# Optimization experiments

Measured on AMD Instinct MI355X. Metric: run time of the kernel, lower is better.

Reference implementation:

```python
import jax, jax.numpy as jnp
import numpy as np
from jax import lax

B, C, H, W, K = 32, 128, 56, 56, 5
CR = C // 4          # reduced channels in weight-gen MLP
CE = 4 * C           # expanded channels
EPS = 1e-6


def setup_inputs() -> dict:
    key = jax.random.key(0)
    ks = jax.random.split(key, 8)
    s = lambda fan: 1.0 / np.sqrt(fan)
    return {
        "x": jax.random.normal(ks[0], (B, C, H, W), jnp.float32),
        "w_fc1": jax.random.normal(ks[1], (CR, C), jnp.float32) * s(C),
        "ln1_w": jnp.ones((CR,), jnp.float32),
        "ln1_b": jnp.zeros((CR,), jnp.float32),
        "w_fc2": jax.random.normal(ks[2], (C * K * K, CR), jnp.float32) * s(CR),
        "ln2_w": jnp.ones((C,), jnp.float32),
        "ln2_b": jnp.zeros((C,), jnp.float32),
        "w_expand": jax.random.normal(ks[3], (CE, C), jnp.float32) * s(C),
        "w_shrink": jax.random.normal(ks[4], (C, CE), jnp.float32) * s(CE),
        "grn_gamma": jax.random.normal(ks[5], (CE,), jnp.float32) * 0.1,
        "grn_beta": jax.random.normal(ks[6], (CE,), jnp.float32) * 0.1,
    }


def _ln(v, w, b, axis):
    u = v.mean(axis, keepdims=True)
    s2 = jnp.square(v - u).mean(axis, keepdims=True)
    return (v - u) * lax.rsqrt(s2 + EPS) * w + b


def reference(x, w_fc1, ln1_w, ln1_b, w_fc2, ln2_w, ln2_b, w_expand, w_shrink,
              grn_gamma, grn_beta):
    b, c, h, w = x.shape
    # ---- dynamic weight generation: pool -> fc1 -> LN -> fc2 ----
    pooled = x.mean((2, 3))                                  # [B, C]
    hdn = pooled @ w_fc1.T                                   # [B, CR]
    hdn = _ln(hdn, ln1_w, ln1_b, axis=-1)                    # channels_first LN over CR
    dyn = hdn @ w_fc2.T                                      # [B, C*K*K]
    dyn_w = dyn.reshape(b * c, 1, K, K)                      # per-sample depthwise kernels
    # ---- per-sample dynamic depthwise conv (groups = B*C) ----
    pad = K // 2
    out = lax.conv_general_dilated(
        x.reshape(1, b * c, h, w), dyn_w,
        window_strides=(1, 1), padding=[(pad, pad), (pad, pad)],
        dimension_numbers=("NCHW", "OIHW", "NCHW"),
        feature_group_count=b * c,
    ).reshape(b, c, h, w)
    # ---- LN (channels_first) over channel dim ----
    u = out.mean(1, keepdims=True)
    s2 = jnp.square(out - u).mean(1, keepdims=True)
    out = (out - u) * lax.rsqrt(s2 + EPS)
    out = ln2_w[None, :, None, None] * out + ln2_b[None, :, None, None]
    # ---- expand 1x1 -> GELU -> GRN -> shrink 1x1 ----
    out = jnp.einsum("bchw,oc->bohw", out, w_expand)         # [B, 4C, H, W]
    out = jax.nn.gelu(out, approximate=False)
    gx = jnp.sqrt(jnp.sum(jnp.square(out), axis=(2, 3), keepdims=True))  # [B,4C,1,1]
    nx = gx / (gx.mean(1, keepdims=True) + EPS)
    g = grn_gamma[None, :, None, None]
    bt = grn_beta[None, :, None, None]
    out = g * (out * nx) + bt + out
    out = jnp.einsum("bohw,co->bchw", out, w_shrink)         # [B, C, H, W]
    return out + x
```

## Files before the change

### kernel.cpp

```cpp
#include <hip/hip_runtime.h>
#include <hip/hip_bf16.h>

#define B_   32
#define C_   128
#define H_   56
#define W_   56
#define HW_  (H_*W_)
#define BHW_ (B_*HW_)
#define K5_  5
#define KK_  25
#define CR_  32
#define CE_  512
#define EPS_ 1e-6f

typedef __hip_bfloat16 bf16;
typedef __attribute__((ext_vector_type(8))) short short8;
typedef __attribute__((ext_vector_type(4))) float f32x4;


__device__ __forceinline__ float wave_reduce_sum(float v) {
#pragma unroll
  for (int off = 32; off > 0; off >>= 1) v += __shfl_down(v, off, 64);
  return v;
}
__device__ __forceinline__ float bf2f(unsigned short u) {
  return __uint_as_float(((unsigned)u) << 16);
}
__device__ __forceinline__ unsigned short f2bf_bits(float f) {
  bf16 h = __float2bfloat16(f);
  unsigned short u;
  __builtin_memcpy(&u, &h, 2);
  return u;
}
__device__ __forceinline__ float fast_gelu(float v) {
  float t = __expf(-1.702f * v);
  return v * __builtin_amdgcn_rcpf(1.0f + t);
}

__global__ __launch_bounds__(256) void prep_kernel(const float* __restrict__ we,
                                                   bf16* __restrict__ weB) {
  int i = blockIdx.x * 256 + threadIdx.x;
  if (i < CE_ * C_) weB[i] = __float2bfloat16(we[i]);
}

__global__ __launch_bounds__(256) void pool_kernel(const float* __restrict__ x,
                                                   float* __restrict__ pooled) {
  int bc = blockIdx.x;
  const float* xp = x + (size_t)bc * HW_;
  float s = 0.f;
  for (int i = threadIdx.x; i < HW_; i += 256) s += xp[i];
  s = wave_reduce_sum(s);
  __shared__ float red[4];
  int lane = threadIdx.x & 63, wid = threadIdx.x >> 6;
  if (lane == 0) red[wid] = s;
  __syncthreads();
  if (threadIdx.x == 0) pooled[bc] = (red[0] + red[1] + red[2] + red[3]) * (1.0f / HW_);
}

__global__ __launch_bounds__(256) void fc_kernel(const float* __restrict__ pooled,
                                                 const float* __restrict__ w_fc1,
                                                 const float* __restrict__ ln1_w,
                                                 const float* __restrict__ ln1_b,
                                                 const float* __restrict__ w_fc2,
                                                 float* __restrict__ dyn) {
  int b = blockIdx.x;
  int tid = threadIdx.x;
  __shared__ float sp[C_];
  __shared__ float sh[CR_];
  __shared__ float shn[CR_];
  __shared__ float stats[2];
  if (tid < C_) sp[tid] = pooled[b * C_ + tid];
  __syncthreads();
  if (tid < CR_) {
    float acc = 0.f;
    const float* wr = w_fc1 + tid * C_;
#pragma unroll 4
    for (int c = 0; c < C_; ++c) acc += sp[c] * wr[c];
    sh[tid] = acc;
  }
  __syncthreads();
  if (tid == 0) {
    float u = 0.f;
    for (int j = 0; j < CR_; ++j) u += sh[j];
    u *= (1.0f / CR_);
    float v = 0.f;
    for (int j = 0; j < CR_; ++j) { float d = sh[j] - u; v += d * d; }
    v *= (1.0f / CR_);
    stats[0] = u;
    stats[1] = rsqrtf(v + EPS_);
  }
  __syncthreads();
  if (tid < CR_) shn[tid] = (sh[tid] - stats[0]) * stats[1] * ln1_w[tid] + ln1_b[tid];
  __syncthreads();
  for (int i = tid; i < C_ * KK_; i += 256) {
    const float* wr = w_fc2 + i * CR_;
    float acc = 0.f;
#pragma unroll
    for (int j = 0; j < CR_; ++j) acc += shn[j] * wr[j];
    dyn[b * (C_ * KK_) + i] = acc;
  }
}

__global__ __launch_bounds__(256) void conv_kernel(const float* __restrict__ x,
                                                   const float* __restrict__ dyn,
                                                   bf16* __restrict__ z) {
  int bc = blockIdx.x;
  int b = bc >> 7;
  int c = bc & 127;
  int tid = threadIdx.x;
  __shared__ float xs[(H_ + 4) * 64];
  __shared__ float wks[KK_];
  {
    int r = tid >> 6;
    int rr = (r < 2) ? r : (56 + r);
    xs[rr * 64 + (tid & 63)] = 0.f;
  }
  if (tid < 224) {
    int r = tid >> 2, q = tid & 3;
    int col = (q < 2) ? q : (56 + q);
    xs[(r + 2) * 64 + col] = 0.f;
  }
  if (tid < KK_) wks[tid] = dyn[b * (C_ * KK_) + c * KK_ + tid];
  const float4* xp4 = reinterpret_cast<const float4*>(x + (size_t)bc * HW_);
  for (int i = tid; i < 784; i += 256) {
    float4 v = xp4[i];
    int h = i / 14, w4 = (i % 14) * 4;
    float* dst = &xs[(h + 2) * 64 + 2 + w4];
    dst[0] = v.x; dst[1] = v.y; dst[2] = v.z; dst[3] = v.w;
  }
  __syncthreads();
  float wr[KK_];
#pragma unroll
  for (int j = 0; j < KK_; ++j) wr[j] = wks[j];
  for (int g = tid; g < 784; g += 256) {
    int h = g / 14;
    int w4 = (g % 14) * 4;
    float a0 = 0.f, a1 = 0.f, a2 = 0.f, a3 = 0.f;
#pragma unroll
    for (int dh = 0; dh < K5_; ++dh) {
      const float* row = &xs[(h + dh) * 64 + w4];
      float4 va = *reinterpret_cast<const float4*>(row);
      float4 vb = *reinterpret_cast<const float4*>(row + 4);
      float v0 = va.x, v1 = va.y, v2 = va.z, v3 = va.w;
      float v4 = vb.x, v5 = vb.y, v6 = vb.z, v7 = vb.w;
      float u0 = wr[dh * 5 + 0], u1 = wr[dh * 5 + 1], u2 = wr[dh * 5 + 2];
      float u3 = wr[dh * 5 + 3], u4 = wr[dh * 5 + 4];
      a0 += v0 * u0 + v1 * u1 + v2 * u2 + v3 * u3 + v4 * u4;
      a1 += v1 * u0 + v2 * u1 + v3 * u2 + v4 * u3 + v5 * u4;
      a2 += v2 * u0 + v3 * u1 + v4 * u2 + v5 * u3 + v6 * u4;
      a3 += v3 * u0 + v4 * u1 + v5 * u2 + v6 * u3 + v7 * u4;
    }
    size_t base = (size_t)bc * HW_ + h * W_ + w4;
    ushort4 pk = make_ushort4(f2bf_bits(a0), f2bf_bits(a1), f2bf_bits(a2), f2bf_bits(a3));
    *reinterpret_cast<ushort4*>(reinterpret_cast<unsigned short*>(z) + base) = pk;
  }
}

__global__ __launch_bounds__(256) void ln_kernel(const bf16* __restrict__ z,
                                                 const float* __restrict__ ln2_w,
                                                 const float* __restrict__ ln2_b,
                                                 bf16* __restrict__ yT) {
  int hw0 = blockIdx.x * 64;
  int b = blockIdx.y;
  int tid = threadIdx.x;
  int wq = tid & 63;
  int cq = tid >> 6;
  __shared__ unsigned short zt[C_][64];
  __shared__ unsigned short yt[64][136];
  __shared__ float redS[4][64];
  __shared__ float redQ[4][64];
  __shared__ float meanArr[64];
  __shared__ float invArr[64];
  float s = 0.f, q = 0.f;
  const unsigned short* zp = reinterpret_cast<const unsigned short*>(z);
#pragma unroll 4
  for (int k = 0; k < 32; ++k) {
    int c = cq * 32 + k;
    unsigned short u = zp[((size_t)(b * C_ + c)) * HW_ + hw0 + wq];
    float v = bf2f(u);
    s += v;
    q += v * v;
    zt[c][wq] = u;
  }
  redS[cq][wq] = s;
  redQ[cq][wq] = q;
  __syncthreads();
  if (cq == 0) {
    float ss = redS[0][wq] + redS[1][wq] + redS[2][wq] + redS[3][wq];
    float qq = redQ[0][wq] + redQ[1][wq] + redQ[2][wq] + redQ[3][wq];
    float m = ss * (1.0f / C_);
    float var = qq * (1.0f / C_) - m * m;
    meanArr[wq] = m;
    invArr[wq] = rsqrtf(fmaxf(var, 0.f) + EPS_);
  }
  __syncthreads();
  float m = meanArr[wq], iv = invArr[wq];
#pragma unroll
  for (int g = 0; g < 4; ++g) {
    unsigned short pk[8];
#pragma unroll
    for (int i = 0; i < 8; ++i) {
      int c = cq * 32 + g * 8 + i;
      float v = bf2f(zt[c][wq]);
      pk[i] = f2bf_bits((v - m) * iv * ln2_w[c] + ln2_b[c]);
    }
    int4 t;
    __builtin_memcpy(&t, pk, 16);
    *reinterpret_cast<int4*>(&yt[wq][cq * 32 + g * 8]) = t;
  }
  __syncthreads();
  unsigned short* yp = reinterpret_cast<unsigned short*>(yT);
#pragma unroll
  for (int i = 0; i < 4; ++i) {
    int t = tid + 256 * i;
    int row = t >> 4, ch = t & 15;
    int4 v = *reinterpret_cast<const int4*>(&yt[row][ch * 8]);
    *reinterpret_cast<int4*>(yp + ((size_t)(b * HW_ + hw0 + row)) * C_ + ch * 8) = v;
  }
}

__global__ __launch_bounds__(256, 4) void expand_mfma(const bf16* __restrict__ yT,
                                                      const bf16* __restrict__ weB,
                                                      bf16* __restrict__ eT,
                                                      float* __restrict__ gx2) {
  int j0 = blockIdx.x * 128;
  int o0 = blockIdx.y * 128;
  int tid = threadIdx.x;
  int lane = tid & 63, wid = tid >> 6;
  int wm = wid >> 1, wn = wid & 1;
  int quad = lane >> 4, l15 = lane & 15;
  __shared__ __align__(16) char smem[128 * 136 * 2];
  short (*As)[40] = reinterpret_cast<short(*)[40]>(&smem[0]);
  short (*Bs)[40] = reinterpret_cast<short(*)[40]>(&smem[10240]);
  f32x4 acc[4][4] = {};
  const short* yTs = reinterpret_cast<const short*>(yT);
  const short* weS = reinterpret_cast<const short*>(weB);
  for (int k0 = 0; k0 < C_; k0 += 32) {
#pragma unroll
    for (int t = tid; t < 512; t += 256) {
      int r = t >> 2, ch = t & 3;
      int4 va = *reinterpret_cast<const int4*>(yTs + (size_t)(j0 + r) * C_ + k0 + ch * 8);
      *reinterpret_cast<int4*>(&As[r][ch * 8]) = va;
      int4 vb = *reinterpret_cast<const int4*>(weS + (size_t)(o0 + r) * C_ + k0 + ch * 8);
      *reinterpret_cast<int4*>(&Bs[r][ch * 8]) = vb;
    }
    __syncthreads();
    short8 a[4], bfr[4];
#pragma unroll
    for (int mf = 0; mf < 4; ++mf)
      a[mf] = *reinterpret_cast<const short8*>(&As[wm * 64 + mf * 16 + l15][quad * 8]);
#pragma unroll
    for (int nf = 0; nf < 4; ++nf)
      bfr[nf] = *reinterpret_cast<const short8*>(&Bs[wn * 64 + nf * 16 + l15][quad * 8]);
#pragma unroll
    for (int mf = 0; mf < 4; ++mf)
#pragma unroll
      for (int nf = 0; nf < 4; ++nf)
        acc[mf][nf] = __builtin_amdgcn_mfma_f32_16x16x32_bf16(a[mf], bfr[nf], acc[mf][nf], 0, 0, 0);
    __syncthreads();
  }
  short (*Es)[136] = reinterpret_cast<short(*)[136]>(&smem[0]);
#pragma unroll
  for (int mf = 0; mf < 4; ++mf) {
    int jm = j0 + wm * 64 + mf * 16;
    int bb = jm / HW_;
    int jrow = wm * 64 + mf * 16 + quad * 4;
#pragma unroll
    for (int nf = 0; nf < 4; ++nf) {
      int oc = wn * 64 + nf * 16 + l15;
      float g2 = 0.f;
#pragma unroll
      for (int r = 0; r < 4; ++r) {
        float ge = fast_gelu(acc[mf][nf][r]);
        g2 += ge * ge;
        Es[jrow + r][oc] = (short)f2bf_bits(ge);
      }
      g2 += __shfl_xor(g2, 16, 64);
      g2 += __shfl_xor(g2, 32, 64);
      if (quad == 0) atomicAdd(&gx2[bb * CE_ + o0 + oc], g2);
    }
  }
  __syncthreads();
  unsigned short* eP = reinterpret_cast<unsigned short*>(eT);
#pragma unroll
  for (int i = 0; i < 8; ++i) {
    int t = tid + 256 * i;
    int row = t >> 4, ch = t & 15;
    int4 v = *reinterpret_cast<const int4*>(&Es[row][ch * 8]);
    *reinterpret_cast<int4*>(eP + (size_t)(j0 + row) * CE_ + o0 + ch * 8) = v;
  }
}

__global__ __launch_bounds__(512) void grn_scale_kernel(const float* __restrict__ gx2,
                                                        const float* __restrict__ gamma,
                                                        float* __restrict__ scale) {
  int b = blockIdx.x;
  int o = threadIdx.x;
  float gx = sqrtf(gx2[b * CE_ + o]);
  float s = wave_reduce_sum(gx);
  __shared__ float red[8];
  __shared__ float meansh;
  int lane = o & 63, wid = o >> 6;
  if (lane == 0) red[wid] = s;
  __syncthreads();
  if (o == 0) {
    float t = 0.f;
    for (int i = 0; i < 8; ++i) t += red[i];
    meansh = t * (1.0f / CE_);
  }
  __syncthreads();
  scale[b * CE_ + o] = 1.0f + gamma[o] * (gx / (meansh + EPS_));
}

__global__ __launch_bounds__(128) void sb_kernel(const float* __restrict__ w_shrink,
                                                 const float* __restrict__ beta,
                                                 float* __restrict__ sb) {
  int c = threadIdx.x;
  float acc = 0.f;
  for (int o = 0; o < CE_; ++o) acc += w_shrink[c * CE_ + o] * beta[o];
  sb[c] = acc;
}

__global__ __launch_bounds__(256) void scale_ws_kernel(const float* __restrict__ ws,
                                                       const float* __restrict__ scale,
                                                       bf16* __restrict__ sws) {
  int c = blockIdx.x;
  int b = blockIdx.y;
  const float* sp = scale + b * CE_;
  const float* wp = ws + (size_t)c * CE_;
  bf16* op = sws + ((size_t)(b * C_ + c)) * CE_;
  for (int i = threadIdx.x; i < CE_; i += 256)
    op[i] = __float2bfloat16(wp[i] * sp[i]);
}

__global__ __launch_bounds__(256, 4) void shrink_mfma(const bf16* __restrict__ eT,
                                                      const bf16* __restrict__ sws,
                                                      const float* __restrict__ sb,
                                                      const float* __restrict__ x,
                                                      float* __restrict__ out) {
  int hw0 = blockIdx.x * 128;
  int b = blockIdx.y;
  int tid = threadIdx.x;
  int lane = tid & 63, wid = tid >> 6;
  int wm = wid >> 1, wn = wid & 1;
  int quad = lane >> 4, l15 = lane & 15;
  __shared__ __align__(16) char smem[64 * 136 * 4];
  short (*As)[40] = reinterpret_cast<short(*)[40]>(&smem[0]);
  short (*Bs)[40] = reinterpret_cast<short(*)[40]>(&smem[10240]);
  f32x4 acc[4][4] = {};
  const short* eS = reinterpret_cast<const short*>(eT) + (size_t)b * HW_ * CE_;
  const short* wsS = reinterpret_cast<const short*>(sws) + (size_t)b * C_ * CE_;
  for (int k0 = 0; k0 < CE_; k0 += 32) {
#pragma unroll
    for (int t = tid; t < 512; t += 256) {
      int r = t >> 2, ch = t & 3;
      int hwc = hw0 + r; if (hwc >= HW_) hwc = HW_ - 1;
      int4 va = *reinterpret_cast<const int4*>(eS + (size_t)hwc * CE_ + k0 + ch * 8);
      *reinterpret_cast<int4*>(&As[r][ch * 8]) = va;
      int4 vb = *reinterpret_cast<const int4*>(wsS + (size_t)r * CE_ + k0 + ch * 8);
      *reinterpret_cast<int4*>(&Bs[r][ch * 8]) = vb;
    }
    __syncthreads();
    short8 a[4], bfr[4];
#pragma unroll
    for (int mf = 0; mf < 4; ++mf)
      a[mf] = *reinterpret_cast<const short8*>(&As[wm * 64 + mf * 16 + l15][quad * 8]);
#pragma unroll
    for (int nf = 0; nf < 4; ++nf)
      bfr[nf] = *reinterpret_cast<const short8*>(&Bs[wn * 64 + nf * 16 + l15][quad * 8]);
#pragma unroll
    for (int mf = 0; mf < 4; ++mf)
#pragma unroll
      for (int nf = 0; nf < 4; ++nf)
        acc[mf][nf] = __builtin_amdgcn_mfma_f32_16x16x32_bf16(a[mf], bfr[nf], acc[mf][nf], 0, 0, 0);
    __syncthreads();
  }
  float (*Ef)[136] = reinterpret_cast<float(*)[136]>(&smem[0]);
#pragma unroll
  for (int phase = 0; phase < 2; ++phase) {
    if (wn == phase) {
#pragma unroll
      for (int mf = 0; mf < 4; ++mf) {
        int hwr = wm * 64 + mf * 16 + quad * 4;
#pragma unroll
        for (int nf = 0; nf < 4; ++nf) {
          int cr = nf * 16 + l15;
          *reinterpret_cast<f32x4*>(&Ef[cr][hwr]) = acc[mf][nf];
        }
      }
    }
    __syncthreads();
#pragma unroll
    for (int i = 0; i < 8; ++i) {
      int t = tid + 256 * i;
      int row = t >> 5, ch = t & 31;
      int hw = hw0 + ch * 4;
      if (hw < HW_) {
        int c = phase * 64 + row;
        size_t base = ((size_t)(b * C_ + c)) * HW_ + hw;
        float add = sb[c];
        f32x4 av = *reinterpret_cast<const f32x4*>(&Ef[row][ch * 4]);
        float4 xv = *reinterpret_cast<const float4*>(x + base);
        float4 ov;
        ov.x = av.x + add + xv.x;
        ov.y = av.y + add + xv.y;
        ov.z = av.z + add + xv.z;
        ov.w = av.w + add + xv.w;
        *reinterpret_cast<float4*>(out + base) = ov;
      }
    }
    __syncthreads();
  }
}

extern "C" void kernel_launch(void* const* d_in, const int* in_sizes, int n_in,
                              void* d_out, int out_size, void* d_ws, size_t ws_size,
                              hipStream_t stream) {
  (void)in_sizes; (void)n_in; (void)out_size; (void)ws_size;
  const float* x        = (const float*)d_in[0];
  const float* w_fc1    = (const float*)d_in[1];
  const float* ln1_w    = (const float*)d_in[2];
  const float* ln1_b    = (const float*)d_in[3];
  const float* w_fc2    = (const float*)d_in[4];
  const float* ln2_w    = (const float*)d_in[5];
  const float* ln2_b    = (const float*)d_in[6];
  const float* w_expand = (const float*)d_in[7];
  const float* w_shrink = (const float*)d_in[8];
  const float* gamma    = (const float*)d_in[9];
  const float* beta     = (const float*)d_in[10];
  float* out = (float*)d_out;

  char* ws = (char*)d_ws;
  float* pooled = (float*)(ws + 0);
  float* dyn    = (float*)(ws + 16384);
  float* gx2    = (float*)(ws + 425984);
  float* scale  = (float*)(ws + 491520);
  float* sb     = (float*)(ws + 557056);
  bf16*  weB    = (bf16*)(ws + 557568);
  bf16*  yT     = (bf16*)(ws + 819712);
  bf16*  sws    = (bf16*)(ws + 819712);
  bf16*  eT     = (bf16*)(ws + 26509824);
  bf16*  z      = eT;

  prep_kernel<<<256, 256, 0, stream>>>(w_expand, weB);
  pool_kernel<<<B_ * C_, 256, 0, stream>>>(x, pooled);
  fc_kernel<<<B_, 256, 0, stream>>>(pooled, w_fc1, ln1_w, ln1_b, w_fc2, dyn);
  conv_kernel<<<B_ * C_, 256, 0, stream>>>(x, dyn, z);
  ln_kernel<<<dim3(49, B_), 256, 0, stream>>>(z, ln2_w, ln2_b, yT);
  hipMemsetAsync(gx2, 0, B_ * CE_ * sizeof(float), stream);
  expand_mfma<<<dim3(784, 4), 256, 0, stream>>>(yT, weB, eT, gx2);
  grn_scale_kernel<<<B_, 512, 0, stream>>>(gx2, gamma, scale);
  sb_kernel<<<1, 128, 0, stream>>>(w_shrink, beta, sb);
  scale_ws_kernel<<<dim3(C_, B_), 256, 0, stream>>>(w_shrink, scale, sws);
  shrink_mfma<<<dim3(25, B_), 256, 0, stream>>>(eT, sws, sb, x, out);
}
```

Baseline: 297.4 us.

## Recompute expand GEMM in fused shrink to avoid materializing expanded activations

Replaces the expand GEMM that wrote the full bf16 expanded tensor with a GEMM pass that only accumulates GRN sum-of-squares. A fused shrink kernel then recomputes the expand GEMM per tile, applies GELU and the GRN scale, stages the result in shared memory and feeds it straight into the shrink GEMM. This removes the large write and read of the 4C expanded intermediate and the per-batch scaled shrink-weight kernel, at the cost of running the expand GEMM twice. Fragments are loaded directly from global memory rather than staged through LDS, and the sb kernel is parallelized across blocks.

```diff
diff --git a/kernel.cpp b/kernel.cpp
--- a/kernel.cpp
+++ b/kernel.cpp
@@ -38,9 +38,12 @@
 }
 
 __global__ __launch_bounds__(256) void prep_kernel(const float* __restrict__ we,
-                                                   bf16* __restrict__ weB) {
+                                                   const float* __restrict__ ws,
+                                                   bf16* __restrict__ weB,
+                                                   bf16* __restrict__ wsB) {
   int i = blockIdx.x * 256 + threadIdx.x;
   if (i < CE_ * C_) weB[i] = __float2bfloat16(we[i]);
+  else              wsB[i - CE_ * C_] = __float2bfloat16(ws[i - CE_ * C_]);
 }
 
 __global__ __launch_bounds__(256) void pool_kernel(const float* __restrict__ x,
@@ -219,75 +222,55 @@
   }
 }
 
-__global__ __launch_bounds__(256, 4) void expand_mfma(const bf16* __restrict__ yT,
-                                                      const bf16* __restrict__ weB,
-                                                      bf16* __restrict__ eT,
-                                                      float* __restrict__ gx2) {
+__global__ __launch_bounds__(256, 2) void gx2_pass(const bf16* __restrict__ yT,
+                                                   const bf16* __restrict__ weB,
+                                                   float* __restrict__ gx2) {
   int j0 = blockIdx.x * 128;
-  int o0 = blockIdx.y * 128;
   int tid = threadIdx.x;
   int lane = tid & 63, wid = tid >> 6;
   int wm = wid >> 1, wn = wid & 1;
   int quad = lane >> 4, l15 = lane & 15;
-  __shared__ __align__(16) char smem[128 * 136 * 2];
-  short (*As)[40] = reinterpret_cast<short(*)[40]>(&smem[0]);
-  short (*Bs)[40] = reinterpret_cast<short(*)[40]>(&smem[10240]);
-  f32x4 acc[4][4] = {};
-  const short* yTs = reinterpret_cast<const short*>(yT);
+  const short* yS = reinterpret_cast<const short*>(yT);
   const short* weS = reinterpret_cast<const short*>(weB);
-  for (int k0 = 0; k0 < C_; k0 += 32) {
-#pragma unroll
-    for (int t = tid; t < 512; t += 256) {
-      int r = t >> 2, ch = t & 3;
-      int4 va = *reinterpret_cast<const int4*>(yTs + (size_t)(j0 + r) * C_ + k0 + ch * 8);
-      *reinterpret_cast<int4*>(&As[r][ch * 8]) = va;
-      int4 vb = *reinterpret_cast<const int4*>(weS + (size_t)(o0 + r) * C_ + k0 + ch * 8);
-      *reinterpret_cast<int4*>(&Bs[r][ch * 8]) = vb;
-    }
-    __syncthreads();
-    short8 a[4], bfr[4];
+  short8 afr[4][4];
+#pragma unroll
+  for (int ks = 0; ks < 4; ++ks)
 #pragma unroll
     for (int mf = 0; mf < 4; ++mf)
-      a[mf] = *reinterpret_cast<const short8*>(&As[wm * 64 + mf * 16 + l15][quad * 8]);
-#pragma unroll
-    for (int nf = 0; nf < 4; ++nf)
-      bfr[nf] = *reinterpret_cast<const short8*>(&Bs[wn * 64 + nf * 16 + l15][quad * 8]);
-#pragma unroll
-    for (int mf = 0; mf < 4; ++mf)
+      afr[ks][mf] = *reinterpret_cast<const short8*>(
+          yS + (size_t)(j0 + wm * 64 + mf * 16 + l15) * C_ + ks * 32 + quad * 8);
+#pragma unroll 1
+  for (int n = 0; n < 4; ++n) {
+    int oc0 = n * 128;
+    f32x4 acc[4][4] = {};
+#pragma unroll
+    for (int ks = 0; ks < 4; ++ks) {
+      short8 bfr[4];
 #pragma unroll
       for (int nf = 0; nf < 4; ++nf)
-        acc[mf][nf] = __builtin_amdgcn_mfma_f32_16x16x32_bf16(a[mf], bfr[nf], acc[mf][nf], 0, 0, 0);
-    __syncthreads();
-  }
-  short (*Es)[136] = reinterpret_cast<short(*)[136]>(&smem[0]);
-#pragma unroll
-  for (int mf = 0; mf < 4; ++mf) {
-    int jm = j0 + wm * 64 + mf * 16;
-    int bb = jm / HW_;
-    int jrow = wm * 64 + mf * 16 + quad * 4;
+        bfr[nf] = *reinterpret_cast<const short8*>(
+            weS + (size_t)(oc0 + wn * 64 + nf * 16 + l15) * C_ + ks * 32 + quad * 8);
+#pragma unroll
+      for (int mf = 0; mf < 4; ++mf)
+#pragma unroll
+        for (int nf = 0; nf < 4; ++nf)
+          acc[mf][nf] = __builtin_amdgcn_mfma_f32_16x16x32_bf16(afr[ks][mf], bfr[nf], acc[mf][nf], 0, 0, 0);
+    }
 #pragma unroll
     for (int nf = 0; nf < 4; ++nf) {
-      int oc = wn * 64 + nf * 16 + l15;
-      float g2 = 0.f;
-#pragma unroll
-      for (int r = 0; r < 4; ++r) {
-        float ge = fast_gelu(acc[mf][nf][r]);
-        g2 += ge * ge;
-        Es[jrow + r][oc] = (short)f2bf_bits(ge);
+      int oc = oc0 + wn * 64 + nf * 16 + l15;
+#pragma unroll
+      for (int mf = 0; mf < 4; ++mf) {
+        int jm = j0 + wm * 64 + mf * 16;
+        int bb = jm / HW_;
+        float g2 = 0.f;
+#pragma unroll
+        for (int r = 0; r < 4; ++r) { float ge = fast_gelu(acc[mf][nf][r]); g2 += ge * ge; }
+        g2 += __shfl_xor(g2, 16, 64);
+        g2 += __shfl_xor(g2, 32, 64);
+        if (quad == 0) atomicAdd(&gx2[bb * CE_ + oc], g2);
       }
-      g2 += __shfl_xor(g2, 16, 64);
-      g2 += __shfl_xor(g2, 32, 64);
-      if (quad == 0) atomicAdd(&gx2[bb * CE_ + o0 + oc], g2);
-    }
-  }
-  __syncthreads();
-  unsigned short* eP = reinterpret_cast<unsigned short*>(eT);
-#pragma unroll
-  for (int i = 0; i < 8; ++i) {
-    int t = tid + 256 * i;
-    int row = t >> 4, ch = t & 15;
-    int4 v = *reinterpret_cast<const int4*>(&Es[row][ch * 8]);
-    *reinterpret_cast<int4*>(eP + (size_t)(j0 + row) * CE_ + o0 + ch * 8) = v;
+    }
   }
 }
 
@@ -312,81 +295,106 @@
   scale[b * CE_ + o] = 1.0f + gamma[o] * (gx / (meansh + EPS_));
 }
 
-__global__ __launch_bounds__(128) void sb_kernel(const float* __restrict__ w_shrink,
+__global__ __launch_bounds__(256) void sb_kernel(const float* __restrict__ w_shrink,
                                                  const float* __restrict__ beta,
                                                  float* __restrict__ sb) {
-  int c = threadIdx.x;
+  int c = blockIdx.x;
+  const float* wp = w_shrink + (size_t)c * CE_;
   float acc = 0.f;
-  for (int o = 0; o < CE_; ++o) acc += w_shrink[c * CE_ + o] * beta[o];
-  sb[c] = acc;
-}
-
-__global__ __launch_bounds__(256) void scale_ws_kernel(const float* __restrict__ ws,
+  for (int o = threadIdx.x; o < CE_; o += 256) acc += wp[o] * beta[o];
+  acc = wave_reduce_sum(acc);
+  __shared__ float red[4];
+  int lane = threadIdx.x & 63, wid = threadIdx.x >> 6;
+  if (lane == 0) red[wid] = acc;
+  __syncthreads();
+  if (threadIdx.x == 0) sb[c] = red[0] + red[1] + red[2] + red[3];
+}
+
+__global__ __launch_bounds__(256, 2) void fused_shrink(const bf16* __restrict__ yT,
+                                                       const bf16* __restrict__ weB,
+                                                       const bf16* __restrict__ wsB,
                                                        const float* __restrict__ scale,
-                                                       bf16* __restrict__ sws) {
-  int c = blockIdx.x;
-  int b = blockIdx.y;
-  const float* sp = scale + b * CE_;
-  const float* wp = ws + (size_t)c * CE_;
-  bf16* op = sws + ((size_t)(b * C_ + c)) * CE_;
-  for (int i = threadIdx.x; i < CE_; i += 256)
-    op[i] = __float2bfloat16(wp[i] * sp[i]);
-}
-
-__global__ __launch_bounds__(256, 4) void shrink_mfma(const bf16* __restrict__ eT,
-                                                      const bf16* __restrict__ sws,
-                                                      const float* __restrict__ sb,
-                                                      const float* __restrict__ x,
-                                                      float* __restrict__ out) {
+                                                       const float* __restrict__ sb,
+                                                       const float* __restrict__ x,
+                                                       float* __restrict__ out) {
   int hw0 = blockIdx.x * 128;
   int b = blockIdx.y;
   int tid = threadIdx.x;
   int lane = tid & 63, wid = tid >> 6;
   int wm = wid >> 1, wn = wid & 1;
   int quad = lane >> 4, l15 = lane & 15;
-  __shared__ __align__(16) char smem[64 * 136 * 4];
-  short (*As)[40] = reinterpret_cast<short(*)[40]>(&smem[0]);
-  short (*Bs)[40] = reinterpret_cast<short(*)[40]>(&smem[10240]);
-  f32x4 acc[4][4] = {};
-  const short* eS = reinterpret_cast<const short*>(eT) + (size_t)b * HW_ * CE_;
-  const short* wsS = reinterpret_cast<const short*>(sws) + (size_t)b * C_ * CE_;
-  for (int k0 = 0; k0 < CE_; k0 += 32) {
-#pragma unroll
-    for (int t = tid; t < 512; t += 256) {
-      int r = t >> 2, ch = t & 3;
-      int hwc = hw0 + r; if (hwc >= HW_) hwc = HW_ - 1;
-      int4 va = *reinterpret_cast<const int4*>(eS + (size_t)hwc * CE_ + k0 + ch * 8);
-      *reinterpret_cast<int4*>(&As[r][ch * 8]) = va;
-      int4 vb = *reinterpret_cast<const int4*>(wsS + (size_t)r * CE_ + k0 + ch * 8);
-      *reinterpret_cast<int4*>(&Bs[r][ch * 8]) = vb;
+  __shared__ __align__(16) char esmem[128 * 136 * 2];
+  short (*Es)[136] = reinterpret_cast<short(*)[136]>(esmem);
+  float (*Ef)[136] = reinterpret_cast<float(*)[136]>(esmem);
+  const short* yS = reinterpret_cast<const short*>(yT) + (size_t)b * HW_ * C_;
+  const short* weS = reinterpret_cast<const short*>(weB);
+  const short* wsS = reinterpret_cast<const short*>(wsB);
+  const float* scp = scale + b * CE_;
+  f32x4 acc2[4][4] = {};
+#pragma unroll 1
+  for (int n = 0; n < 4; ++n) {
+    int oc0 = n * 128;
+    f32x4 acc1[4][4] = {};
+#pragma unroll
+    for (int ks = 0; ks < 4; ++ks) {
+      short8 afr[4], bfr[4];
+#pragma unroll
+      for (int mf = 0; mf < 4; ++mf) {
+        int hwc = hw0 + wm * 64 + mf * 16 + l15;
+        if (hwc >= HW_) hwc = HW_ - 1;
+        afr[mf] = *reinterpret_cast<const short8*>(yS + (size_t)hwc * C_ + ks * 32 + quad * 8);
+      }
+#pragma unroll
+      for (int nf = 0; nf < 4; ++nf)
+        bfr[nf] = *reinterpret_cast<const short8*>(
+            weS + (size_t)(oc0 + wn * 64 + nf * 16 + l15) * C_ + ks * 32 + quad * 8);
+#pragma unroll
+      for (int mf = 0; mf < 4; ++mf)
+#pragma unroll
+        for (int nf = 0; nf < 4; ++nf)
+          acc1[mf][nf] = __builtin_amdgcn_mfma_f32_16x16x32_bf16(afr[mf], bfr[nf], acc1[mf][nf], 0, 0, 0);
     }
     __syncthreads();
-    short8 a[4], bfr[4];
-#pragma unroll
-    for (int mf = 0; mf < 4; ++mf)
-      a[mf] = *reinterpret_cast<const short8*>(&As[wm * 64 + mf * 16 + l15][quad * 8]);
-#pragma unroll
-    for (int nf = 0; nf < 4; ++nf)
-      bfr[nf] = *reinterpret_cast<const short8*>(&Bs[wn * 64 + nf * 16 + l15][quad * 8]);
-#pragma unroll
-    for (int mf = 0; mf < 4; ++mf)
+#pragma unroll
+    for (int nf = 0; nf < 4; ++nf) {
+      int ocl = wn * 64 + nf * 16 + l15;
+      float sc = scp[oc0 + ocl];
+#pragma unroll
+      for (int mf = 0; mf < 4; ++mf) {
+        int row = wm * 64 + mf * 16 + quad * 4;
+#pragma unroll
+        for (int r = 0; r < 4; ++r)
+          Es[row + r][ocl] = (short)f2bf_bits(fast_gelu(acc1[mf][nf][r]) * sc);
+      }
+    }
+    __syncthreads();
+#pragma unroll
+    for (int kk = 0; kk < 4; ++kk) {
+      short8 a2[4], b2[4];
+#pragma unroll
+      for (int mf = 0; mf < 4; ++mf)
+        a2[mf] = *reinterpret_cast<const short8*>(&Es[wm * 64 + mf * 16 + l15][kk * 32 + quad * 8]);
 #pragma unroll
       for (int nf = 0; nf < 4; ++nf)
-        acc[mf][nf] = __builtin_amdgcn_mfma_f32_16x16x32_bf16(a[mf], bfr[nf], acc[mf][nf], 0, 0, 0);
-    __syncthreads();
-  }
-  float (*Ef)[136] = reinterpret_cast<float(*)[136]>(&smem[0]);
-#pragma unroll
+        b2[nf] = *reinterpret_cast<const short8*>(
+            wsS + (size_t)(wn * 64 + nf * 16 + l15) * CE_ + oc0 + kk * 32 + quad * 8);
+#pragma unroll
+      for (int mf = 0; mf < 4; ++mf)
+#pragma unroll
+        for (int nf = 0; nf < 4; ++nf)
+          acc2[mf][nf] = __builtin_amdgcn_mfma_f32_16x16x32_bf16(a2[mf], b2[nf], acc2[mf][nf], 0, 0, 0);
+    }
+  }
+  __syncthreads();
+#pragma unroll 1
   for (int phase = 0; phase < 2; ++phase) {
     if (wn == phase) {
 #pragma unroll
       for (int mf = 0; mf < 4; ++mf) {
         int hwr = wm * 64 + mf * 16 + quad * 4;
 #pragma unroll
-        for (int nf = 0; nf < 4; ++nf) {
-          int cr = nf * 16 + l15;
-          *reinterpret_cast<f32x4*>(&Ef[cr][hwr]) = acc[mf][nf];
-        }
+        for (int nf = 0; nf < 4; ++nf)
+          *reinterpret_cast<f32x4*>(&Ef[nf * 16 + l15][hwr]) = acc2[mf][nf];
       }
     }
     __syncthreads();
@@ -437,20 +445,18 @@
   float* scale  = (float*)(ws + 491520);
   float* sb     = (float*)(ws + 557056);
   bf16*  weB    = (bf16*)(ws + 557568);
+  bf16*  wsB    = (bf16*)(ws + 688640);
   bf16*  yT     = (bf16*)(ws + 819712);
-  bf16*  sws    = (bf16*)(ws + 819712);
-  bf16*  eT     = (bf16*)(ws + 26509824);
-  bf16*  z      = eT;
-
-  prep_kernel<<<256, 256, 0, stream>>>(w_expand, weB);
+  bf16*  z      = (bf16*)(ws + 26509824);
+
+  prep_kernel<<<512, 256, 0, stream>>>(w_expand, w_shrink, weB, wsB);
+  hipMemsetAsync(gx2, 0, B_ * CE_ * sizeof(float), stream);
+  sb_kernel<<<C_, 256, 0, stream>>>(w_shrink, beta, sb);
   pool_kernel<<<B_ * C_, 256, 0, stream>>>(x, pooled);
   fc_kernel<<<B_, 256, 0, stream>>>(pooled, w_fc1, ln1_w, ln1_b, w_fc2, dyn);
   conv_kernel<<<B_ * C_, 256, 0, stream>>>(x, dyn, z);
   ln_kernel<<<dim3(49, B_), 256, 0, stream>>>(z, ln2_w, ln2_b, yT);
-  hipMemsetAsync(gx2, 0, B_ * CE_ * sizeof(float), stream);
-  expand_mfma<<<dim3(784, 4), 256, 0, stream>>>(yT, weB, eT, gx2);
+  gx2_pass<<<784, 256, 0, stream>>>(yT, weB, gx2);
   grn_scale_kernel<<<B_, 512, 0, stream>>>(gx2, gamma, scale);
-  sb_kernel<<<1, 128, 0, stream>>>(w_shrink, beta, sb);
-  scale_ws_kernel<<<dim3(C_, B_), 256, 0, stream>>>(w_shrink, scale, sws);
-  shrink_mfma<<<dim3(25, B_), 256, 0, stream>>>(eT, sws, sb, x, out);
-}
+  fused_shrink<<<dim3(25, B_), 256, 0, stream>>>(yT, weB, wsB, scale, sb, x, out);
+}
```

Measured after the change: 340.9 us. 14.6% more time.
